# Performance work log

Measured on AMD Instinct MI355X. Metric: run time of the kernel, lower is better.

## Reference

```python
import jax, jax.numpy as jnp
import numpy as np

N_NODES = 100000
N_EDGES = 1600000
D = 128


def sage_conv(x, src, dst, W_l, b_l, W_r):
    # mean aggregation of neighbor features: messages flow src -> dst
    msgs = x[src]                                           # [E, D] gather
    agg = jax.ops.segment_sum(msgs, dst, num_segments=x.shape[0])  # [N, D]
    deg = jax.ops.segment_sum(jnp.ones((src.shape[0],), x.dtype), dst,
                              num_segments=x.shape[0])       # [N]
    agg = agg / jnp.maximum(deg, 1.0)[:, None]
    # PyG SAGEConv: lin_l(aggregated) + lin_r(root); bias lives in lin_l
    return agg @ W_l.T + b_l + x @ W_r.T


def setup_inputs() -> dict:
    key = jax.random.key(0)
    ks = jax.random.split(key, 8)
    s = 1.0 / np.sqrt(D)
    return {
        "x": jax.random.normal(ks[0], (N_NODES, D), dtype=jnp.float32),
        "edge_index": jax.random.randint(ks[1], (2, N_EDGES), 0, N_NODES, dtype=jnp.int64),
        "W1_l": jax.random.normal(ks[2], (D, D), dtype=jnp.float32) * s,
        "b1": jnp.zeros((D,), dtype=jnp.float32),
        "W1_r": jax.random.normal(ks[3], (D, D), dtype=jnp.float32) * s,
        "W2_l": jax.random.normal(ks[4], (D, D), dtype=jnp.float32) * s,
        "b2": jnp.zeros((D,), dtype=jnp.float32),
        "W2_r": jax.random.normal(ks[5], (D, D), dtype=jnp.float32) * s,
    }


def reference(x, edge_index, W1_l, b1, W1_r, W2_l, b2, W2_r):
    src, dst = edge_index[0], edge_index[1]
    h = jax.nn.relu(sage_conv(x, src, dst, W1_l, b1, W1_r))
    out = sage_conv(h, src, dst, W2_l, b2, W2_r)
    return out
```

## Files before the change

### kernel.cpp

```cpp
#include <hip/hip_runtime.h>
#include <cstdint>
#include <cstddef>

#define D 128

typedef unsigned short ushort_t;
typedef unsigned int uint_t;
typedef __attribute__((ext_vector_type(8))) short bf16x8;
typedef __attribute__((ext_vector_type(4))) float f32x4;

static __device__ __forceinline__ unsigned short f2bf(float f) {
    unsigned int u = __float_as_uint(f);
    u = (u + 0x7FFFu + ((u >> 16) & 1u)) >> 16;
    return (unsigned short)u;
}
static __device__ __forceinline__ float bf_lo(uint_t v) {
    return __uint_as_float(v << 16);
}
static __device__ __forceinline__ float bf_hi(uint_t v) {
    return __uint_as_float(v & 0xFFFF0000u);
}

static __device__ __forceinline__ void cast8(const float* __restrict__ s,
                                             ushort_t* __restrict__ d) {
    float4 a = *(const float4*)s;
    float4 b = *(const float4*)(s + 4);
    uint4 o;
    o.x = (uint_t)f2bf(a.x) | ((uint_t)f2bf(a.y) << 16);
    o.y = (uint_t)f2bf(a.z) | ((uint_t)f2bf(a.w) << 16);
    o.z = (uint_t)f2bf(b.x) | ((uint_t)f2bf(b.y) << 16);
    o.w = (uint_t)f2bf(b.z) | ((uint_t)f2bf(b.w) << 16);
    *(uint4*)d = o;
}


__global__ __launch_bounds__(256) void front_fused(
    const int* __restrict__ dst, int* __restrict__ bhist, int E, int EB,
    const float* __restrict__ x, ushort_t* __restrict__ xb, long nx, int CX,
    const float* __restrict__ W1l, const float* __restrict__ W1r,
    const float* __restrict__ W2l, const float* __restrict__ W2r,
    ushort_t* __restrict__ W1lb, ushort_t* __restrict__ W1rb,
    ushort_t* __restrict__ W2lb, ushort_t* __restrict__ W2rb) {
    __shared__ int lh[512];
    int b = blockIdx.x, t = threadIdx.x;
    if (b < EB) {
        lh[t] = 0;
        lh[t + 256] = 0;
        __syncthreads();
        int base = b * 4096;
#pragma unroll
        for (int i = 0; i < 16; ++i) {
            int e = base + i * 256 + t;
            if (e < E) atomicAdd(&lh[dst[e] >> 8], 1);
        }
        __syncthreads();
        if (lh[t]) atomicAdd(&bhist[t], lh[t]);
        if (lh[t + 256]) atomicAdd(&bhist[t + 256], lh[t + 256]);
    } else if (b < EB + CX) {
        long i = ((long)(b - EB) * 256 + t) * 8;
        if (i < nx) cast8(x + i, xb + i);
    } else {
        int bb = b - EB - CX;
        int arr = bb >> 3;
        long i = ((long)(bb & 7) * 256 + t) * 8;
        const float* s = (arr == 0) ? W1l : (arr == 1) ? W1r
                       : (arr == 2) ? W2l : W2r;
        ushort_t* d = (arr == 0) ? W1lb : (arr == 1) ? W1rb
                    : (arr == 2) ? W2lb : W2rb;
        cast8(s + i, d + i);
    }
}


__global__ __launch_bounds__(512) void bkt_scan(const int* __restrict__ bhist,
                                                int* __restrict__ boff,
                                                int* __restrict__ bcur,
                                                int* __restrict__ row_ptr,
                                                int N, int E) {
    __shared__ int s[512];
    int t = threadIdx.x;
    int v = bhist[t];
    s[t] = v;
    __syncthreads();
    for (int off = 1; off < 512; off <<= 1) {
        int u = (t >= off) ? s[t - off] : 0;
        __syncthreads();
        s[t] += u;
        __syncthreads();
    }
    int ex = s[t] - v;
    boff[t] = ex;
    bcur[t] = ex;
    if (t == 511) boff[512] = s[511];
    if (t == 0) row_ptr[N] = E;
}

__global__ __launch_bounds__(256) void bkt_scatter(const int* __restrict__ src,
                                                   const int* __restrict__ dst,
                                                   int* __restrict__ bcur,
                                                   int* __restrict__ ebuf, int E) {
    __shared__ int lh[512];
    __shared__ int lofs[512];
    __shared__ int gb[512];
    __shared__ int sv[4096];
    __shared__ unsigned short sb[4096];
    int t = threadIdx.x;
    lh[t] = 0;
    lh[t + 256] = 0;
    __syncthreads();
    int base = blockIdx.x * 4096;
    unsigned pk[16];
#pragma unroll
    for (int i = 0; i < 16; ++i) {
        int e = base + i * 256 + t;
        unsigned p = 0xFFFFFFFFu;
        if (e < E) {
            int d = dst[e];
            int bkt = d >> 8;
            int r = atomicAdd(&lh[bkt], 1);
            p = ((unsigned)r << 17) | ((unsigned)bkt << 8) | (unsigned)(d & 255);
        }
        pk[i] = p;
    }
    __syncthreads();
    int a0 = lh[2 * t], a1 = lh[2 * t + 1];
    int ps = a0 + a1;
    gb[t] = ps;
    __syncthreads();
    for (int off = 1; off < 256; off <<= 1) {
        int u = (t >= off) ? gb[t - off] : 0;
        __syncthreads();
        gb[t] += u;
        __syncthreads();
    }
    int inc = gb[t];
    int exb = inc - ps;
    __syncthreads();
    lofs[2 * t] = exb;
    lofs[2 * t + 1] = exb + a0;
    if (a0) gb[2 * t] = atomicAdd(&bcur[2 * t], a0);
    if (a1) gb[2 * t + 1] = atomicAdd(&bcur[2 * t + 1], a1);
    __syncthreads();
#pragma unroll
    for (int i = 0; i < 16; ++i) {
        int e = base + i * 256 + t;
        if (e < E) {
            unsigned p = pk[i];
            int bkt = (p >> 8) & 511;
            int r = (int)(p >> 17);
            int pos = lofs[bkt] + r;
            sv[pos] = src[e] | ((int)(p & 255) << 20);
            sb[pos] = (unsigned short)bkt;
        }
    }
    __syncthreads();
    int cnt = min(E - base, 4096);
    for (int i = t; i < cnt; i += 256) {
        int b2 = sb[i];
        ebuf[gb[b2] + (i - lofs[b2])] = sv[i];
    }
}

__global__ __launch_bounds__(256) void bkt_build(const int* __restrict__ ebuf,
                                                 const int* __restrict__ boff,
                                                 int* __restrict__ row_ptr,
                                                 int* __restrict__ csr, int N) {
    __shared__ int lcnt[256];
    __shared__ int lofs[256];
    __shared__ int lcur[256];
    int t = threadIdx.x;
    int b = blockIdx.x;
    int base = b << 8;
    int ebeg = boff[b], eend = boff[b + 1];
    lcnt[t] = 0;
    __syncthreads();
    for (int e = ebeg + t; e < eend; e += 256)
        atomicAdd(&lcnt[((unsigned)ebuf[e]) >> 20], 1);
    __syncthreads();
    int v = lcnt[t];
    lofs[t] = v;
    __syncthreads();
    for (int off = 1; off < 256; off <<= 1) {
        int u = (t >= off) ? lofs[t - off] : 0;
        __syncthreads();
        lofs[t] += u;
        __syncthreads();
    }
    int ex = lofs[t] - v;
    __syncthreads();
    lofs[t] = ex;
    lcur[t] = 0;
    if (base + t < N) row_ptr[base + t] = ebeg + ex;
    __syncthreads();
    for (int e = ebeg + t; e < eend; e += 256) {
        int u = ebuf[e];
        int d = ((unsigned)u) >> 20;
        int r = atomicAdd(&lcur[d], 1);
        csr[ebeg + lofs[d] + r] = u & 0xFFFFF;
    }
}


static __device__ __forceinline__ void acc8(uint4 v, float a[8]) {
    a[0] += bf_lo(v.x); a[1] += bf_hi(v.x);
    a[2] += bf_lo(v.y); a[3] += bf_hi(v.y);
    a[4] += bf_lo(v.z); a[5] += bf_hi(v.z);
    a[6] += bf_lo(v.w); a[7] += bf_hi(v.w);
}

static __device__ __forceinline__ uint4 grow(const ushort_t* __restrict__ xin,
                                             int s, int l16) {
    unsigned off = ((unsigned)s << 8) | ((unsigned)l16 << 4);
    return *(const uint4*)((const char*)xin + off);
}

__global__ __launch_bounds__(256) void agg_b_kernel(const ushort_t* __restrict__ xin,
                                                    const int* __restrict__ csr,
                                                    const int* __restrict__ row_ptr,
                                                    ushort_t* __restrict__ aggb, int N) {
    int node = blockIdx.x * 4 + (threadIdx.x >> 6);
    if (node >= N) return;
    int lane = threadIdx.x & 63;
    int g = lane >> 4;
    int l16 = lane & 15;
    int beg = row_ptr[node], end = row_ptr[node + 1];
    int deg = end - beg;
    float a[8] = {0.f, 0.f, 0.f, 0.f, 0.f, 0.f, 0.f, 0.f};

    if (deg > 0) {
        int deg64 = min(deg, 64);
        int myidx = csr[beg + min(lane, deg - 1)];
        int e = 0;
        for (; e + 16 <= deg64; e += 16) {
            int s0 = __shfl(myidx, e + g);
            int s1 = __shfl(myidx, e + 4 + g);
            int s2 = __shfl(myidx, e + 8 + g);
            int s3 = __shfl(myidx, e + 12 + g);
            uint4 v0 = grow(xin, s0, l16);
            uint4 v1 = grow(xin, s1, l16);
            uint4 v2 = grow(xin, s2, l16);
            uint4 v3 = grow(xin, s3, l16);
            acc8(v0, a); acc8(v1, a); acc8(v2, a); acc8(v3, a);
        }
        if (e + 8 <= deg64) {
            int s0 = __shfl(myidx, e + g);
            int s1 = __shfl(myidx, e + 4 + g);
            uint4 v0 = grow(xin, s0, l16);
            uint4 v1 = grow(xin, s1, l16);
            acc8(v0, a); acc8(v1, a);
            e += 8;
        }
        if (e + 4 <= deg64) {
            int s0 = __shfl(myidx, e + g);
            uint4 v0 = grow(xin, s0, l16);
            acc8(v0, a);
            e += 4;
        }
        if (e < deg64) {
            int ee = min(e + g, deg64 - 1);
            int s = __shfl(myidx, ee);
            uint4 v = grow(xin, s, l16);
            if (e + g < deg64) acc8(v, a);
        }
        for (int e2 = 64; e2 < deg; e2 += 4) {
            int s = csr[beg + min(e2 + g, deg - 1)];
            uint4 v = grow(xin, s, l16);
            if (e2 + g < deg) acc8(v, a);
        }
    }

#pragma unroll
    for (int i = 0; i < 8; ++i) {
        a[i] += __shfl_xor(a[i], 16);
        a[i] += __shfl_xor(a[i], 32);
    }
    if (g == 0) {
        float inv = 1.0f / fmaxf((float)deg, 1.0f);
        uint4 o;
        o.x = (uint_t)f2bf(a[0] * inv) | ((uint_t)f2bf(a[1] * inv) << 16);
        o.y = (uint_t)f2bf(a[2] * inv) | ((uint_t)f2bf(a[3] * inv) << 16);
        o.z = (uint_t)f2bf(a[4] * inv) | ((uint_t)f2bf(a[5] * inv) << 16);
        o.w = (uint_t)f2bf(a[6] * inv) | ((uint_t)f2bf(a[7] * inv) << 16);
        unsigned off = ((unsigned)node << 8) | ((unsigned)l16 << 4);
        *(uint4*)((char*)aggb + off) = o;
    }
}


__global__ __launch_bounds__(256) void gemm_mfma(const ushort_t* __restrict__ Aagg,
                                                 const ushort_t* __restrict__ Ax,
                                                 const ushort_t* __restrict__ Wl,
                                                 const ushort_t* __restrict__ Wr,
                                                 const float* __restrict__ bias,
                                                 ushort_t* __restrict__ out_bf,
                                                 float* __restrict__ out_f32,
                                                 int N, int relu_bf) {
    __shared__ ushort_t sA[128 * 32];
    __shared__ ushort_t sW[128 * 32];
    int tid = threadIdx.x;
    int wave = tid >> 6, lane = tid & 63;
    int quad = lane >> 4, l15 = lane & 15;
    int wm = wave & 1, wc = wave >> 1;
    int n0 = blockIdx.x * 128;
    int sr = tid >> 2;
    int sseg = (tid & 3) * 8;

    f32x4 acc[4][4];
#pragma unroll
    for (int mt = 0; mt < 4; ++mt)
#pragma unroll
        for (int nt = 0; nt < 4; ++nt) acc[mt][nt] = (f32x4){0.f, 0.f, 0.f, 0.f};

    int ga0 = min(n0 + sr, N - 1);
    int ga1 = min(n0 + sr + 64, N - 1);

#pragma unroll
    for (int c = 0; c < 8; ++c) {
        const ushort_t* Ab = (c < 4) ? Aagg : Ax;
        const ushort_t* Wb = (c < 4) ? Wl : Wr;
        int koff = (c & 3) * 32 + sseg;
        bf16x8 va0 = *(const bf16x8*)(Ab + (size_t)ga0 * D + koff);
        bf16x8 va1 = *(const bf16x8*)(Ab + (size_t)ga1 * D + koff);
        bf16x8 vw0 = *(const bf16x8*)(Wb + (size_t)sr * D + koff);
        bf16x8 vw1 = *(const bf16x8*)(Wb + (size_t)(sr + 64) * D + koff);
        __syncthreads();
        *(bf16x8*)&sA[sr * 32 + sseg] = va0;
        *(bf16x8*)&sA[(sr + 64) * 32 + sseg] = va1;
        *(bf16x8*)&sW[sr * 32 + sseg] = vw0;
        *(bf16x8*)&sW[(sr + 64) * 32 + sseg] = vw1;
        __syncthreads();

        bf16x8 af[4], wf[4];
#pragma unroll
        for (int mt = 0; mt < 4; ++mt)
            af[mt] = *(const bf16x8*)&sA[(wm * 64 + mt * 16 + l15) * 32 + quad * 8];
#pragma unroll
        for (int nt = 0; nt < 4; ++nt)
            wf[nt] = *(const bf16x8*)&sW[(wc * 64 + nt * 16 + l15) * 32 + quad * 8];
#pragma unroll
        for (int mt = 0; mt < 4; ++mt)
#pragma unroll
            for (int nt = 0; nt < 4; ++nt)
                acc[mt][nt] = __builtin_amdgcn_mfma_f32_16x16x32_bf16(
                    af[mt], wf[nt], acc[mt][nt], 0, 0, 0);
    }

#pragma unroll
    for (int mt = 0; mt < 4; ++mt) {
#pragma unroll
        for (int nt = 0; nt < 4; ++nt) {
            int col = wc * 64 + nt * 16 + l15;
            float bv = bias[col];
#pragma unroll
            for (int reg = 0; reg < 4; ++reg) {
                int row = n0 + wm * 64 + mt * 16 + quad * 4 + reg;
                if (row < N) {
                    float v = acc[mt][nt][reg] + bv;
                    if (relu_bf) {
                        v = fmaxf(v, 0.f);
                        out_bf[(size_t)row * D + col] = f2bf(v);
                    } else {
                        out_f32[(size_t)row * D + col] = v;
                    }
                }
            }
        }
    }
}


extern "C" void kernel_launch(void* const* d_in, const int* in_sizes, int n_in,
                              void* d_out, int out_size, void* d_ws, size_t ws_size,
                              hipStream_t stream) {
    const float* x   = (const float*)d_in[0];
    const int*   ei  = (const int*)d_in[1];
    const float* W1l = (const float*)d_in[2];
    const float* b1  = (const float*)d_in[3];
    const float* W1r = (const float*)d_in[4];
    const float* W2l = (const float*)d_in[5];
    const float* b2  = (const float*)d_in[6];
    const float* W2r = (const float*)d_in[7];
    float* out = (float*)d_out;

    int N = in_sizes[0] / D;
    int E = in_sizes[1] / 2;
    const int* src = ei;
    const int* dst = ei + E;

    char* ws = (char*)d_ws;
    size_t off = 0;
    auto take = [&](size_t bytes) -> char* {
        char* p = ws + off;
        off += (bytes + 255) & ~(size_t)255;
        return p;
    };
    int*      row_ptr = (int*)take((size_t)(N + 1) * sizeof(int));
    int*      bhist   = (int*)take((size_t)(512 + 512 + 513) * sizeof(int));
    int*      bcur    = bhist + 512;
    int*      boff    = bhist + 1024;
    int*      ebuf    = (int*)take((size_t)E * sizeof(int));
    int*      csr     = (int*)take((size_t)E * sizeof(int));
    ushort_t* xb      = (ushort_t*)take((size_t)N * D * sizeof(ushort_t));
    ushort_t* hb      = (ushort_t*)take((size_t)N * D * sizeof(ushort_t));
    ushort_t* aggb    = (ushort_t*)take((size_t)N * D * sizeof(ushort_t));
    ushort_t* W1lb    = (ushort_t*)take((size_t)D * D * sizeof(ushort_t));
    ushort_t* W1rb    = (ushort_t*)take((size_t)D * D * sizeof(ushort_t));
    ushort_t* W2lb    = (ushort_t*)take((size_t)D * D * sizeof(ushort_t));
    ushort_t* W2rb    = (ushort_t*)take((size_t)D * D * sizeof(ushort_t));
    (void)ws_size;
    (void)n_in;
    (void)out_size;

    hipMemsetAsync(bhist, 0, 1024 * sizeof(int), stream);

    int NB = (N + 255) / 256;
    int EB = (E + 4095) / 4096;
    long nx = (long)N * D;
    int CX = (int)((nx / 8 + 255) / 256);

    front_fused<<<EB + CX + 32, 256, 0, stream>>>(
        dst, bhist, E, EB, x, xb, nx, CX,
        W1l, W1r, W2l, W2r, W1lb, W1rb, W2lb, W2rb);
    bkt_scan<<<1, 512, 0, stream>>>(bhist, boff, bcur, row_ptr, N, E);
    bkt_scatter<<<EB, 256, 0, stream>>>(src, dst, bcur, ebuf, E);
    bkt_build<<<NB, 256, 0, stream>>>(ebuf, boff, row_ptr, csr, N);

    int ablocks = (N + 3) / 4;
    int gblocks = (N + 127) / 128;

    agg_b_kernel<<<ablocks, 256, 0, stream>>>(xb, csr, row_ptr, aggb, N);
    gemm_mfma<<<gblocks, 256, 0, stream>>>(aggb, xb, W1lb, W1rb, b1, hb, nullptr, N, 1);

    agg_b_kernel<<<ablocks, 256, 0, stream>>>(hb, csr, row_ptr, aggb, N);
    gemm_mfma<<<gblocks, 256, 0, stream>>>(aggb, hb, W2lb, W2rb, b2, nullptr, out, N, 0);
}
```

Baseline: 336.4 us.

## Split aggregation and GEMM into halves and overlap in a fused mid kernel

Rows are split at a 128-aligned midpoint. The first half of the aggregation runs alone. A fused kernel then runs the second-half aggregation alongside the first-half GEMM, and a final kernel handles the second-half GEMM. This lets gather-bound and MFMA-bound work share the GPU. Each aggregation wave now processes two nodes with interleaved loads, which raises memory-level parallelism. The cost is an extra launch per layer, more register pressure, and possible load imbalance between the co-scheduled block types.

```diff
diff --git a/kernel.cpp b/kernel.cpp
--- a/kernel.cpp
+++ b/kernel.cpp
@@ -214,80 +214,105 @@
     return *(const uint4*)((const char*)xin + off);
 }
 
-__global__ __launch_bounds__(256) void agg_b_kernel(const ushort_t* __restrict__ xin,
-                                                    const int* __restrict__ csr,
-                                                    const int* __restrict__ row_ptr,
-                                                    ushort_t* __restrict__ aggb, int N) {
-    int node = blockIdx.x * 4 + (threadIdx.x >> 6);
-    if (node >= N) return;
+static __device__ __forceinline__ void agg_store(ushort_t* __restrict__ aggb,
+                                                 int node, int l16,
+                                                 const float a[8], int deg) {
+    float inv = 1.0f / fmaxf((float)deg, 1.0f);
+    uint4 o;
+    o.x = (uint_t)f2bf(a[0] * inv) | ((uint_t)f2bf(a[1] * inv) << 16);
+    o.y = (uint_t)f2bf(a[2] * inv) | ((uint_t)f2bf(a[3] * inv) << 16);
+    o.z = (uint_t)f2bf(a[4] * inv) | ((uint_t)f2bf(a[5] * inv) << 16);
+    o.w = (uint_t)f2bf(a[6] * inv) | ((uint_t)f2bf(a[7] * inv) << 16);
+    unsigned off = ((unsigned)node << 8) | ((unsigned)l16 << 4);
+    *(uint4*)((char*)aggb + off) = o;
+}
+
+static __device__ __forceinline__ void agg_body(int bid, int base, int cnt,
+                                                const ushort_t* __restrict__ xin,
+                                                const int* __restrict__ csr,
+                                                const int* __restrict__ row_ptr,
+                                                ushort_t* __restrict__ aggb) {
+    int wave = threadIdx.x >> 6;
     int lane = threadIdx.x & 63;
     int g = lane >> 4;
     int l16 = lane & 15;
-    int beg = row_ptr[node], end = row_ptr[node + 1];
-    int deg = end - beg;
-    float a[8] = {0.f, 0.f, 0.f, 0.f, 0.f, 0.f, 0.f, 0.f};
-
-    if (deg > 0) {
-        int deg64 = min(deg, 64);
-        int myidx = csr[beg + min(lane, deg - 1)];
-        int e = 0;
-        for (; e + 16 <= deg64; e += 16) {
-            int s0 = __shfl(myidx, e + g);
-            int s1 = __shfl(myidx, e + 4 + g);
-            int s2 = __shfl(myidx, e + 8 + g);
-            int s3 = __shfl(myidx, e + 12 + g);
-            uint4 v0 = grow(xin, s0, l16);
-            uint4 v1 = grow(xin, s1, l16);
-            uint4 v2 = grow(xin, s2, l16);
-            uint4 v3 = grow(xin, s3, l16);
-            acc8(v0, a); acc8(v1, a); acc8(v2, a); acc8(v3, a);
-        }
-        if (e + 8 <= deg64) {
-            int s0 = __shfl(myidx, e + g);
-            int s1 = __shfl(myidx, e + 4 + g);
-            uint4 v0 = grow(xin, s0, l16);
-            uint4 v1 = grow(xin, s1, l16);
-            acc8(v0, a); acc8(v1, a);
-            e += 8;
-        }
-        if (e + 4 <= deg64) {
-            int s0 = __shfl(myidx, e + g);
-            uint4 v0 = grow(xin, s0, l16);
-            acc8(v0, a);
-            e += 4;
-        }
-        if (e < deg64) {
-            int ee = min(e + g, deg64 - 1);
-            int s = __shfl(myidx, ee);
-            uint4 v = grow(xin, s, l16);
-            if (e + g < deg64) acc8(v, a);
-        }
-        for (int e2 = 64; e2 < deg; e2 += 4) {
-            int s = csr[beg + min(e2 + g, deg - 1)];
-            uint4 v = grow(xin, s, l16);
-            if (e2 + g < deg) acc8(v, a);
-        }
-    }
-
+    int p = bid * 8 + wave * 2;
+    if (p >= cnt) return;
+    int node0 = base + p;
+    int node1 = base + min(p + 1, cnt - 1);
+    int b0 = row_ptr[node0];
+    int deg0 = row_ptr[node0 + 1] - b0;
+    int b1 = row_ptr[node1];
+    int deg1 = row_ptr[node1 + 1] - b1;
+    int d0 = min(deg0, 64), d1 = min(deg1, 64);
+    int i0 = (deg0 > 0) ? csr[b0 + min(lane, deg0 - 1)] : 0;
+    int i1 = (deg1 > 0) ? csr[b1 + min(lane, deg1 - 1)] : 0;
+    int c0 = max(d0 - 1, 0), c1 = max(d1 - 1, 0);
+    float a0[8] = {0.f, 0.f, 0.f, 0.f, 0.f, 0.f, 0.f, 0.f};
+    float a1[8] = {0.f, 0.f, 0.f, 0.f, 0.f, 0.f, 0.f, 0.f};
+    int mm = max(d0, d1);
+    for (int e = 0; e < mm; e += 16) {
+        bool do0 = (e < d0), do1 = (e < d1);
+        uint4 v0[4], v1[4];
+        if (do0) {
+#pragma unroll
+            for (int q = 0; q < 4; ++q) {
+                int s = __shfl(i0, min(e + 4 * q + g, c0));
+                v0[q] = grow(xin, s, l16);
+            }
+        }
+        if (do1) {
+#pragma unroll
+            for (int q = 0; q < 4; ++q) {
+                int s = __shfl(i1, min(e + 4 * q + g, c1));
+                v1[q] = grow(xin, s, l16);
+            }
+        }
+        if (do0) {
+#pragma unroll
+            for (int q = 0; q < 4; ++q)
+                if (e + 4 * q + g < d0) acc8(v0[q], a0);
+        }
+        if (do1) {
+#pragma unroll
+            for (int q = 0; q < 4; ++q)
+                if (e + 4 * q + g < d1) acc8(v1[q], a1);
+        }
+    }
+    for (int e2 = 64; e2 < deg0; e2 += 4) {
+        int s = csr[b0 + min(e2 + g, deg0 - 1)];
+        uint4 v = grow(xin, s, l16);
+        if (e2 + g < deg0) acc8(v, a0);
+    }
+    for (int e2 = 64; e2 < deg1; e2 += 4) {
+        int s = csr[b1 + min(e2 + g, deg1 - 1)];
+        uint4 v = grow(xin, s, l16);
+        if (e2 + g < deg1) acc8(v, a1);
+    }
 #pragma unroll
     for (int i = 0; i < 8; ++i) {
-        a[i] += __shfl_xor(a[i], 16);
-        a[i] += __shfl_xor(a[i], 32);
+        a0[i] += __shfl_xor(a0[i], 16);
+        a1[i] += __shfl_xor(a1[i], 16);
+        a0[i] += __shfl_xor(a0[i], 32);
+        a1[i] += __shfl_xor(a1[i], 32);
     }
     if (g == 0) {
-        float inv = 1.0f / fmaxf((float)deg, 1.0f);
-        uint4 o;
-        o.x = (uint_t)f2bf(a[0] * inv) | ((uint_t)f2bf(a[1] * inv) << 16);
-        o.y = (uint_t)f2bf(a[2] * inv) | ((uint_t)f2bf(a[3] * inv) << 16);
-        o.z = (uint_t)f2bf(a[4] * inv) | ((uint_t)f2bf(a[5] * inv) << 16);
-        o.w = (uint_t)f2bf(a[6] * inv) | ((uint_t)f2bf(a[7] * inv) << 16);
-        unsigned off = ((unsigned)node << 8) | ((unsigned)l16 << 4);
-        *(uint4*)((char*)aggb + off) = o;
-    }
-}
-
-
-__global__ __launch_bounds__(256) void gemm_mfma(const ushort_t* __restrict__ Aagg,
+        agg_store(aggb, node0, l16, a0, deg0);
+        agg_store(aggb, node1, l16, a1, deg1);
+    }
+}
+
+__global__ __launch_bounds__(256) void agg_k(const ushort_t* __restrict__ xin,
+                                             const int* __restrict__ csr,
+                                             const int* __restrict__ row_ptr,
+                                             ushort_t* __restrict__ aggb,
+                                             int base, int cnt) {
+    agg_body(blockIdx.x, base, cnt, xin, csr, row_ptr, aggb);
+}
+
+
+static __device__ __forceinline__ void gemm_body(int tile, int rbase,
+                                                 const ushort_t* __restrict__ Aagg,
                                                  const ushort_t* __restrict__ Ax,
                                                  const ushort_t* __restrict__ Wl,
                                                  const ushort_t* __restrict__ Wr,
@@ -301,7 +326,7 @@
     int wave = tid >> 6, lane = tid & 63;
     int quad = lane >> 4, l15 = lane & 15;
     int wm = wave & 1, wc = wave >> 1;
-    int n0 = blockIdx.x * 128;
+    int n0 = rbase + tile * 128;
     int sr = tid >> 2;
     int sseg = (tid & 3) * 8;
 
@@ -365,6 +390,31 @@
                 }
             }
         }
+    }
+}
+
+__global__ __launch_bounds__(256) void gemm_k(const ushort_t* __restrict__ Aagg,
+                                              const ushort_t* __restrict__ Ax,
+                                              const ushort_t* __restrict__ Wl,
+                                              const ushort_t* __restrict__ Wr,
+                                              const float* __restrict__ bias,
+                                              ushort_t* __restrict__ out_bf,
+                                              float* __restrict__ out_f32,
+                                              int rbase, int N, int relu_bf) {
+    gemm_body(blockIdx.x, rbase, Aagg, Ax, Wl, Wr, bias, out_bf, out_f32, N, relu_bf);
+}
+
+__global__ __launch_bounds__(256) void mid_fused(
+    const ushort_t* __restrict__ xin, const int* __restrict__ csr,
+    const int* __restrict__ row_ptr, ushort_t* __restrict__ aggb,
+    const ushort_t* __restrict__ Wl, const ushort_t* __restrict__ Wr,
+    const float* __restrict__ bias, ushort_t* __restrict__ out_bf,
+    float* __restrict__ out_f32, int H, int N, int relu_bf, int aggBlocks) {
+    if ((int)blockIdx.x < aggBlocks) {
+        agg_body(blockIdx.x, H, N - H, xin, csr, row_ptr, aggb);
+    } else {
+        gemm_body(blockIdx.x - aggBlocks, 0, aggb, xin, Wl, Wr, bias,
+                  out_bf, out_f32, N, relu_bf);
     }
 }
 
@@ -425,12 +475,26 @@
     bkt_scatter<<<EB, 256, 0, stream>>>(src, dst, bcur, ebuf, E);
     bkt_build<<<NB, 256, 0, stream>>>(ebuf, boff, row_ptr, csr, N);
 
-    int ablocks = (N + 3) / 4;
-    int gblocks = (N + 127) / 128;
-
-    agg_b_kernel<<<ablocks, 256, 0, stream>>>(xb, csr, row_ptr, aggb, N);
-    gemm_mfma<<<gblocks, 256, 0, stream>>>(aggb, xb, W1lb, W1rb, b1, hb, nullptr, N, 1);
-
-    agg_b_kernel<<<ablocks, 256, 0, stream>>>(hb, csr, row_ptr, aggb, N);
-    gemm_mfma<<<gblocks, 256, 0, stream>>>(aggb, hb, W2lb, W2rb, b2, nullptr, out, N, 0);
-}
+    int H = ((N / 2 + 127) / 128) * 128;
+    if (H > N) H = N;
+    int aggA = (H + 7) / 8;
+    int aggB = (N - H + 7) / 8;
+    int gemA = H / 128;
+    int gemB = (N - H + 127) / 128;
+
+    if (aggA) agg_k<<<aggA, 256, 0, stream>>>(xb, csr, row_ptr, aggb, 0, H);
+    if (aggB + gemA)
+        mid_fused<<<aggB + gemA, 256, 0, stream>>>(xb, csr, row_ptr, aggb,
+                                                   W1lb, W1rb, b1, hb, nullptr,
+                                                   H, N, 1, aggB);
+    if (gemB) gemm_k<<<gemB, 256, 0, stream>>>(aggb, xb, W1lb, W1rb, b1,
+                                               hb, nullptr, H, N, 1);
+
+    if (aggA) agg_k<<<aggA, 256, 0, stream>>>(hb, csr, row_ptr, aggb, 0, H);
+    if (aggB + gemA)
+        mid_fused<<<aggB + gemA, 256, 0, stream>>>(hb, csr, row_ptr, aggb,
+                                                   W2lb, W2rb, b2, nullptr, out,
+                                                   H, N, 0, aggB);
+    if (gemB) gemm_k<<<gemB, 256, 0, stream>>>(aggb, hb, W2lb, W2rb, b2,
+                                               nullptr, out, H, N, 0);
+}
```

New measurement: 367.0 us. 1.09x slower.
